# Optimization experiments

Measured on AMD Instinct MI355X. Metric: run time of the kernel, lower is better.

Reference implementation:

```python
import jax, jax.numpy as jnp
import numpy as np

D = 512      # input_dim == encoder d_model
E = 512      # embedding_dim (codebook dim)
V = 8192     # num_embeddings
NC = 1       # num_codebooks
L = 6        # encoder layers
H = 8        # heads
F = 2048     # ffn dim
HD = D // H
EPS = 1e-5


def layernorm(x, s, b):
    m = jnp.mean(x, -1, keepdims=True)
    v = jnp.mean((x - m) ** 2, -1, keepdims=True)
    return (x - m) * jax.lax.rsqrt(v + EPS) * s + b


def sinusoidal_pe(T):
    pos = np.arange(T, dtype=np.float32)[:, None]
    i = np.arange(0, D, 2, dtype=np.float32)[None, :]
    ang = pos / np.power(10000.0, i / D)
    pe = np.zeros((T, D), np.float32)
    pe[:, 0::2] = np.sin(ang)
    pe[:, 1::2] = np.cos(ang)
    return jnp.asarray(pe)


def setup_inputs():
    key = jax.random.key(0)
    ks = jax.random.split(key, 12)
    B, T = 8, 1024
    xs = jax.random.normal(ks[0], (B, T, D), jnp.float32)
    xs_lens = (T // 2 + jax.random.randint(ks[1], (B,), 0, T // 2)).astype(jnp.int32)
    mask_indices = jax.random.uniform(ks[2], (B, T)) < 0.12  # span-mask surrogate
    sc = lambda k, shape, s=0.02: jax.random.normal(k, shape, jnp.float32) * s
    return {
        "xs": xs, "xs_lens": xs_lens, "mask_indices": mask_indices,
        "W_embed": sc(ks[3], (D, D), D ** -0.5),
        "ln1_s": jnp.ones((L, D)), "ln1_b": jnp.zeros((L, D)),
        "Wqkv": sc(ks[4], (L, D, 3 * D)), "Wo": sc(ks[5], (L, D, D)),
        "ln2_s": jnp.ones((L, D)), "ln2_b": jnp.zeros((L, D)),
        "W1": sc(ks[6], (L, D, F)), "W2": sc(ks[7], (L, F, D)),
        "an_s": jnp.ones((D,)), "an_b": jnp.zeros((D,)),
        "iln_s": jnp.ones((D,)), "iln_b": jnp.zeros((D,)),
        "mask_emb": sc(ks[8], (D,), 0.1),
        "top_n_out": sc(ks[9], (NC, D, V)),
        "projection": sc(ks[10], (D, E), (2.0 / (D + E)) ** 0.5),  # xavier_normal, frozen
        "embeddings": jax.random.normal(ks[11], (NC, E, V), jnp.float32),  # frozen codebook
    }


def encoder_blocks(x, pad_mask, ln1_s, ln1_b, Wqkv, Wo, ln2_s, ln2_b, W1, W2, an_s, an_b):
    B, T, _ = x.shape
    attn_bias = jnp.where(pad_mask, 0.0, -1e9)[:, None, None, :]  # [B,1,1,T]

    def layer(x, p):
        l1s, l1b, wqkv, wo, l2s, l2b, w1, w2 = p
        h = layernorm(x, l1s, l1b)
        q, k, v = jnp.split(h @ wqkv, 3, axis=-1)
        q = q.reshape(B, T, H, HD)
        k = k.reshape(B, T, H, HD)
        v = v.reshape(B, T, H, HD)
        scores = jnp.einsum('bqhd,bkhd->bhqk', q, k) * (HD ** -0.5) + attn_bias
        o = jnp.einsum('bhqk,bkhd->bqhd', jax.nn.softmax(scores, axis=-1), v)
        x = x + o.reshape(B, T, D) @ wo
        h = layernorm(x, l2s, l2b)
        x = x + jax.nn.relu(h @ w1) @ w2
        return x, None

    x, _ = jax.lax.scan(layer, x, (ln1_s, ln1_b, Wqkv, Wo, ln2_s, ln2_b, W1, W2))
    return layernorm(x, an_s, an_b)


def nearest_ids(x, iln_s, iln_b, projection, embeddings):
    # layernorm -> projection -> squared-distance argmin per codebook
    B, T, _ = x.shape
    z = layernorm(x, iln_s, iln_b) @ projection        # [B,T,E]
    flat = z.reshape(-1, E)                            # [N,E]
    d = (jnp.sum(flat ** 2, 1)[None, :, None]
         + jnp.sum(embeddings ** 2, 1)[:, None, :]
         - 2.0 * jnp.einsum('ne,gev->gnv', flat, embeddings))  # [NC,N,V]
    return jnp.argmin(d, -1).T.reshape(B, T, NC)


def reference(xs, xs_lens, mask_indices, W_embed, ln1_s, ln1_b, Wqkv, Wo, ln2_s, ln2_b,
              W1, W2, an_s, an_b, iln_s, iln_b, mask_emb, top_n_out, projection, embeddings):
    B, T, _ = xs.shape
    pad_mask = jnp.arange(T)[None, :] < xs_lens[:, None]              # [B,T]
    x = xs @ W_embed + sinusoidal_pe(T)[None]                         # encoder.embed
    target_ids = nearest_ids(x, iln_s, iln_b, projection, embeddings)  # [B,T,NC]
    masked_xs = jnp.where(mask_indices[..., None], mask_emb, x)
    out = encoder_blocks(masked_xs, pad_mask, ln1_s, ln1_b, Wqkv, Wo,
                         ln2_s, ln2_b, W1, W2, an_s, an_b)            # [B,T,D]
    logits = jnp.einsum('btd,gdv->bgtv', out, top_n_out)              # [B,NC,T,V]
    lsm = jax.nn.log_softmax(logits, axis=-1)
    tgt = jnp.transpose(target_ids, (0, 2, 1))                        # [B,NC,T]
    ent = -jnp.take_along_axis(lsm, tgt[..., None], axis=-1)[..., 0]  # [B,NC,T]
    m = (pad_mask & mask_indices).astype(jnp.float32)                 # [B,T]
    loss = jnp.sum(ent * m[:, None, :]) / (jnp.sum(m) * NC)
    return loss
```

## Files before the change

### kernel.cpp

```cpp
#include <hip/hip_runtime.h>
#include <hip/hip_bf16.h>

#define D_ 512
#define T_ 1024
#define B_ 8
#define H_ 8
#define F_ 2048
#define V_ 8192
#define L_ 6
#define NTOK 8192
#define EPS_ 1e-5f
#define NCAP 2048

typedef short short8 __attribute__((ext_vector_type(8)));
typedef float floatx4 __attribute__((ext_vector_type(4)));

__device__ __forceinline__ float bf2f(unsigned short u) {
  union { unsigned int i; float f; } v; v.i = ((unsigned int)u) << 16; return v.f;
}
__device__ __forceinline__ unsigned short f2bf(float f) {
  unsigned int u = __float_as_uint(f);
  return (unsigned short)((u + 0x7fffu + ((u >> 16) & 1u)) >> 16);
}
__device__ __forceinline__ float ldf(const void* p, long long i, int bf) {
  if (bf) return bf2f(((const unsigned short*)p)[i]);
  return ((const float*)p)[i];
}
__device__ __forceinline__ void ld16(const unsigned short* g, unsigned short* l) {
  __builtin_amdgcn_global_load_lds(
      (const __attribute__((address_space(1))) unsigned int*)g,
      (__attribute__((address_space(3))) unsigned int*)l, 16, 0, 0);
}
__device__ __forceinline__ unsigned int fkey(float f) {
  unsigned int u = __float_as_uint(f);
  return (u & 0x80000000u) ? ~u : (u ^ 0x80000000u);
}

__global__ void detect_kernel(const unsigned int* xsw, const unsigned int* mw, int* flags) {
  __shared__ int cnt[256];
  __shared__ int m01[256], mlo[256], mhi[256];
  int tid = threadIdx.x;
  int c = 0;
  for (int t = tid; t < 1024; t += 256) {
    unsigned int lo = xsw[t] & 0xffffu;
    int ok;
    if (lo == 0u) ok = 1;
    else { unsigned int e = (lo >> 7) & 0xffu; ok = (e >= 90u && e <= 140u); }
    c += ok;
  }
  int n01 = 0, lo38 = 0, hi38 = 0;
  for (int t = tid; t < 2048; t += 256) {
    unsigned int w = mw[t];
    if (w > 1u) n01 = 1;
    if ((w & 0xffffu) == 0x3f80u) lo38 = 1;
    if ((w >> 16) == 0x3f80u) hi38 = 1;
  }
  cnt[tid] = c; m01[tid] = n01; mlo[tid] = lo38; mhi[tid] = hi38;
  __syncthreads();
  for (int s = 128; s > 0; s >>= 1) {
    if (tid < s) {
      cnt[tid] += cnt[tid + s];
      m01[tid] |= m01[tid + s]; mlo[tid] |= mlo[tid + s]; mhi[tid] |= mhi[tid + s];
    }
    __syncthreads();
  }
  if (tid == 0) {
    flags[0] = (cnt[0] > 700) ? 1 : 0;
    int fmt;
    if (!m01[0]) fmt = 0;
    else if (mlo[0]) fmt = 2;
    else if (mhi[0]) fmt = 3;
    else fmt = 1;
    flags[1] = fmt;
  }
}

__global__ void conv_all_kernel(const void* d4, const void* d5, const void* d8,
                                const void* d9, const void* d12, const void* d13,
                                const void* d14, const void* d15, const void* d16,
                                float* P, const int* flags) {
  int i = blockIdx.x * 256 + threadIdx.x;
  if (i >= 14848) return;
  int bf = flags[0];
  const void* src; int off;
  if (i < 3072) { src = d4; off = 0; }
  else if (i < 6144) { src = d5; off = 3072; }
  else if (i < 9216) { src = d8; off = 6144; }
  else if (i < 12288) { src = d9; off = 9216; }
  else if (i < 12800) { src = d12; off = 12288; }
  else if (i < 13312) { src = d13; off = 12800; }
  else if (i < 13824) { src = d14; off = 13312; }
  else if (i < 14336) { src = d15; off = 13824; }
  else { src = d16; off = 14336; }
  P[i] = ldf(src, i - off, bf);
}

__global__ void convb_kernel(const void* src, unsigned short* dst, int n, const int* flags) {
  int i = blockIdx.x * 256 + threadIdx.x;
  if (i < n) {
    if (flags[0]) dst[i] = ((const unsigned short*)src)[i];
    else dst[i] = f2bf(((const float*)src)[i]);
  }
}

__global__ __launch_bounds__(256) void trans_kernel(const void* src, unsigned short* dst,
                                                    int K, int N, const int* flags) {
  int bf = flags[0];
  __shared__ unsigned short tile[32][33];
  int n0 = blockIdx.x * 32, k0 = blockIdx.y * 32, batch = blockIdx.z;
  long long sbase = (long long)batch * K * N;
  long long dbase = (long long)batch * N * K;
  int c = threadIdx.x & 31, r8 = threadIdx.x >> 5;
#pragma unroll
  for (int rr = 0; rr < 4; ++rr) {
    int r = r8 + rr * 8;
    tile[r][c] = f2bf(ldf(src, sbase + (long long)(k0 + r) * N + n0 + c, bf));
  }
  __syncthreads();
#pragma unroll
  for (int rr = 0; rr < 4; ++rr) {
    int nn = r8 + rr * 8;
    dst[dbase + (long long)(n0 + nn) * K + k0 + c] = tile[c][nn];
  }
}

__global__ __launch_bounds__(256) void trans_big_kernel(const void* top, const void* emb,
                                                        unsigned short* TOPT, unsigned short* EMBT,
                                                        float* en, const int* flags) {
  int bf = flags[0];
  __shared__ unsigned short tile[32][33];
  int n0 = blockIdx.x * 32, k0 = blockIdx.y * 32, z = blockIdx.z;
  const void* src = z ? emb : top;
  unsigned short* dst = z ? EMBT : TOPT;
  int c = threadIdx.x & 31, r8 = threadIdx.x >> 5;
#pragma unroll
  for (int rr = 0; rr < 4; ++rr) {
    int r = r8 + rr * 8;
    tile[r][c] = f2bf(ldf(src, (long long)(k0 + r) * V_ + n0 + c, bf));
  }
  __syncthreads();
#pragma unroll
  for (int rr = 0; rr < 4; ++rr) {
    int nn = r8 + rr * 8;
    dst[(long long)(n0 + nn) * D_ + k0 + c] = tile[c][nn];
  }
  if (z == 1 && threadIdx.x < 32) {
    int nn = threadIdx.x;
    float s = 0.f;
#pragma unroll
    for (int r = 0; r < 32; ++r) { float x = bf2f(tile[r][nn]); s += x * x; }
    atomicAdd(&en[n0 + nn], s);
  }
}

__global__ void prep_kernel(const void* mask, const int* lens, int* maski, float* mcomb,
                            int* idx, int* cnt, const int* flags) {
  int i = blockIdx.x * 256 + threadIdx.x;
  if (i >= NTOK) return;
  int fmt = flags[1];
  int mi;
  if (fmt == 0) mi = ((const int*)mask)[i] != 0;
  else if (fmt == 1) mi = ((const unsigned char*)mask)[i] != 0;
  else if (fmt == 2) mi = ((const unsigned short*)mask)[i] != 0;
  else mi = ((const float*)mask)[i] != 0.f;
  int b = i >> 10, t = i & (T_ - 1);
  int act = mi && (t < lens[b]);
  maski[i] = mi;
  mcomb[i] = act ? 1.f : 0.f;
  if (act) {
    int p = atomicAdd(cnt, 1);
    if (p < NCAP) idx[p] = i;
  }
}

#define BK 32

template<int BN>
__device__ __forceinline__ void stage_tile(const unsigned short* A, long long ga0, long long ga1,
                                           const unsigned short* BT, long long gb0, long long gb1,
                                           int k0, unsigned short (*Ab)[BK],
                                           unsigned short (*Bb)[BK], int wave, int sw8) {
  ld16(A + ga0 + k0 + sw8, &Ab[wave * 32][0]);
  ld16(A + ga1 + k0 + sw8, &Ab[wave * 32 + 16][0]);
  if constexpr (BN == 128) {
    ld16(BT + gb0 + k0 + sw8, &Bb[wave * 32][0]);
    ld16(BT + gb1 + k0 + sw8, &Bb[wave * 32 + 16][0]);
  } else {
    ld16(BT + gb0 + k0 + sw8, &Bb[wave * 16][0]);
  }
}

template<int BN>
__device__ __forceinline__ void mfma_pipe(const unsigned short* A, long long ga0, long long ga1,
                                          const unsigned short* BT, int n0, int Kdim,
                                          int kofs, int Klen,
                                          unsigned short (*As)[BK], unsigned short (*Bs)[BK],
                                          floatx4 (*acc)[BN / 32], int tid) {
  constexpr int NB = BN / 32;
  int wave = tid >> 6, lane = tid & 63;
  int r16 = lane >> 2, c16 = lane & 3;
  int lrow = lane & 15, quad = lane >> 4;
  int wm = (wave & 1) * 64, wn = (wave >> 1) * (BN / 2);
  int NT = Klen / BK;
  int sw8 = (c16 ^ ((r16 >> 1) & 3)) * 8;
  int swr = (quad ^ ((lrow >> 1) & 3)) * 8;
  long long gb0, gb1 = 0;
  if constexpr (BN == 128) {
    gb0 = (long long)(n0 + wave * 32 + r16) * Kdim;
    gb1 = gb0 + 16LL * Kdim;
  } else {
    gb0 = (long long)(n0 + wave * 16 + r16) * Kdim;
  }
  ga0 += kofs; ga1 += kofs; gb0 += kofs; gb1 += kofs;
  stage_tile<BN>(A, ga0, ga1, BT, gb0, gb1, 0, As, Bs, wave, sw8);
  stage_tile<BN>(A, ga0, ga1, BT, gb0, gb1, BK, As + 128, Bs + BN, wave, sw8);
  int cur = 0, nxt = 2;
  for (int t = 0; t < NT; ++t) {
    if (t == NT - 1) {
      asm volatile("s_waitcnt vmcnt(0)" ::: "memory");
    } else {
      if constexpr (BN == 128) asm volatile("s_waitcnt vmcnt(4)" ::: "memory");
      else                     asm volatile("s_waitcnt vmcnt(3)" ::: "memory");
    }
    __builtin_amdgcn_s_barrier();
    if (t + 2 < NT)
      stage_tile<BN>(A, ga0, ga1, BT, gb0, gb1, (t + 2) * BK,
                     As + nxt * 128, Bs + nxt * BN, wave, sw8);
    unsigned short (*Ac)[BK] = As + cur * 128;
    unsigned short (*Bc)[BK] = Bs + cur * BN;
    short8 af[4], bfr[NB];
#pragma unroll
    for (int i = 0; i < 4; ++i) af[i] = *(const short8*)&Ac[wm + i * 16 + lrow][swr];
#pragma unroll
    for (int j = 0; j < NB; ++j) bfr[j] = *(const short8*)&Bc[wn + j * 16 + lrow][swr];
#pragma unroll
    for (int i = 0; i < 4; ++i)
#pragma unroll
      for (int j = 0; j < NB; ++j)
        acc[i][j] = __builtin_amdgcn_mfma_f32_16x16x32_bf16(af[i], bfr[j], acc[i][j], 0, 0, 0);
    cur = (cur == 2) ? 0 : cur + 1;
    nxt = (nxt == 2) ? 0 : nxt + 1;
  }
  __syncthreads();
}

__global__ __launch_bounds__(256) void mgemm_kernel(const unsigned short* A,
    const unsigned short* BT, long long boff, unsigned short* Cb, int Ndim, int Kdim) {
  __shared__ __align__(16) unsigned short As[3 * 128][BK];
  __shared__ __align__(16) unsigned short Bs[3 * 128][BK];
  int tid = threadIdx.x;
  int bid = blockIdx.x;
  int m0 = (bid & 63) * 128, n0 = (bid >> 6) * 128;
  int wave = tid >> 6, lane = tid & 63;
  int wm = (wave & 1) * 64, wn = (wave >> 1) * 64;
  int lrow = lane & 15, quad = lane >> 4;
  int r16 = lane >> 2;
  floatx4 acc[4][4];
#pragma unroll
  for (int i = 0; i < 4; ++i)
#pragma unroll
    for (int j = 0; j < 4; ++j) acc[i][j] = (floatx4){0.f, 0.f, 0.f, 0.f};
  long long ga0 = (long long)(m0 + wave * 32 + r16) * Kdim;
  long long ga1 = ga0 + 16LL * Kdim;
  mfma_pipe<128>(A, ga0, ga1, BT + boff, n0, Kdim, 0, Kdim, As, Bs, acc, tid);
#pragma unroll
  for (int i = 0; i < 4; ++i) {
    int mb = m0 + wm + i * 16 + quad * 4;
#pragma unroll
    for (int j = 0; j < 4; ++j) {
      int ncol = n0 + wn + j * 16 + lrow;
#pragma unroll
      for (int r = 0; r < 4; ++r)
        Cb[(long long)(mb + r) * Ndim + ncol] = f2bf(fmaxf(acc[i][j][r], 0.f));
    }
  }
}

__global__ __launch_bounds__(256) void mgemm64_kernel(const unsigned short* A,
    const unsigned short* BT, long long boff, float* Cf, unsigned short* Cb,
    int Ndim, int Kdim, int mode) {
  __shared__ __align__(16) unsigned short As[3 * 128][BK];
  __shared__ __align__(16) unsigned short Bs[3 * 64][BK];
  int tid = threadIdx.x;
  int bid = blockIdx.x;
  int m0 = (bid & 63) * 128;
  int nt = bid >> 6;
  int n0, kofs, Klen;
  if (mode == 5) { n0 = (nt & 7) * 64; kofs = (nt >> 3) * (Kdim >> 1); Klen = Kdim >> 1; }
  else { n0 = nt * 64; kofs = 0; Klen = Kdim; }
  int wave = tid >> 6, lane = tid & 63;
  int r16 = lane >> 2;
  int wm = (wave & 1) * 64, wn = (wave >> 1) * 32;
  int lrow = lane & 15, quad = lane >> 4;
  floatx4 acc[4][2];
#pragma unroll
  for (int i = 0; i < 4; ++i)
#pragma unroll
    for (int j = 0; j < 2; ++j) acc[i][j] = (floatx4){0.f, 0.f, 0.f, 0.f};
  long long ga0 = (long long)(m0 + wave * 32 + r16) * Kdim;
  long long ga1 = ga0 + 16LL * Kdim;
  mfma_pipe<64>(A, ga0, ga1, BT + boff, n0, Kdim, kofs, Klen, As, Bs, acc, tid);
#pragma unroll
  for (int i = 0; i < 4; ++i) {
    int mb = m0 + wm + i * 16 + quad * 4;
#pragma unroll
    for (int j = 0; j < 2; ++j) {
      int ncol = n0 + wn + j * 16 + lrow;
#pragma unroll
      for (int r = 0; r < 4; ++r) {
        int m = mb + r;
        long long idx = (long long)m * Ndim + ncol;
        float v = acc[i][j][r];
        if (mode == 1) Cf[idx] += v;
        else if (mode == 5) atomicAdd(&Cf[idx], v);
        else if (mode == 4) Cb[idx] = f2bf(v);
        else if (mode == 3) {
          int t = m & (T_ - 1);
          float freq = __expf(-(float)(ncol & ~1) * (9.210340371976184f / (float)D_));
          float ang = (float)t * freq;
          v += (ncol & 1) ? cosf(ang) : sinf(ang);
          Cf[idx] = v;
        } else Cf[idx] = v;
      }
    }
  }
}

__global__ __launch_bounds__(256) void qkvgemm_kernel(const unsigned short* A,
    const unsigned short* BT, long long boff, unsigned short* QB,
    unsigned short* KSg, unsigned short* VTSg) {
  __shared__ __align__(16) union {
    struct { unsigned short As[3 * 128][BK]; unsigned short Bs[3 * 128][BK]; } s;
    unsigned short T[128][136];
  } sm;
  int tid = threadIdx.x;
  int bid = blockIdx.x;
  int m0 = (bid & 63) * 128;
  int nt = bid >> 6;
  int n0 = nt * 128;
  int wave = tid >> 6, lane = tid & 63;
  int wm = (wave & 1) * 64, wn = (wave >> 1) * 64;
  int lrow = lane & 15, quad = lane >> 4;
  int r16 = lane >> 2;
  floatx4 acc[4][4];
#pragma unroll
  for (int i = 0; i < 4; ++i)
#pragma unroll
    for (int j = 0; j < 4; ++j) acc[i][j] = (floatx4){0.f, 0.f, 0.f, 0.f};
  long long ga0 = (long long)(m0 + wave * 32 + r16) * D_;
  long long ga1 = ga0 + 16LL * D_;
  mfma_pipe<128>(A, ga0, ga1, BT + boff, n0, D_, 0, D_, sm.s.As, sm.s.Bs, acc, tid);
  int b = m0 >> 10, tt = (m0 >> 7) & 7;
  if (nt < 4) {
#pragma unroll
    for (int i = 0; i < 4; ++i) {
      int mb = m0 + wm + i * 16 + quad * 4;
#pragma unroll
      for (int j = 0; j < 4; ++j) {
        int ncol = n0 + wn + j * 16 + lrow;
#pragma unroll
        for (int r = 0; r < 4; ++r)
          QB[(long long)(mb + r) * 512 + ncol] = f2bf(acc[i][j][r]);
      }
    }
  } else if (nt < 8) {
#pragma unroll
    for (int i = 0; i < 4; ++i)
#pragma unroll
      for (int j = 0; j < 4; ++j)
#pragma unroll
        for (int r = 0; r < 4; ++r)
          sm.T[wm + i * 16 + quad * 4 + r][wn + j * 16 + lrow] = f2bf(acc[i][j][r]);
    __syncthreads();
    int tk = tid & 127, hg0 = tid >> 7;
#pragma unroll
    for (int p = 0; p < 8; ++p) {
      int hg = p * 2 + hg0;
      int h2 = hg >> 3, g = hg & 7;
      uint4 u = *(const uint4*)&sm.T[tk][h2 * 64 + g * 8];
      int headg = (nt - 4) * 2 + h2;
      long long dst = (((((long long)(b * 8 + headg)) * 8 + tt) * 8 + g) * 128 + tk) * 8;
      *(uint4*)&KSg[dst] = u;
    }
  } else {
#pragma unroll
    for (int i = 0; i < 4; ++i)
#pragma unroll
      for (int j = 0; j < 4; ++j)
#pragma unroll
        for (int r = 0; r < 4; ++r)
          sm.T[wn + j * 16 + lrow][wm + i * 16 + quad * 4 + r] = f2bf(acc[i][j][r]);
    __syncthreads();
    int col = tid & 127, gh = tid >> 7;
    int h2 = col >> 6, ch = col & 63;
    int headg = (nt - 8) * 2 + h2;
    long long base = ((((long long)(b * 8 + headg)) * 8 + tt) * 16);
#pragma unroll
    for (int p = 0; p < 8; ++p) {
      int g = p * 2 + gh;
      uint4 u = *(const uint4*)&sm.T[col][g * 8];
      long long dst = ((base + g) * 64 + ch) * 8;
      *(uint4*)&VTSg[dst] = u;
    }
  }
}

__global__ __launch_bounds__(256) void fattn_kernel(const unsigned short* QB,
    const unsigned short* KSg, const unsigned short* VTSg, const int* lens,
    unsigned short* ao) {
  __shared__ __align__(16) unsigned short Ps[64 * 128];
  int blk = blockIdx.x;
  int swz = (blk & 7) * 128 + (blk >> 3);
  int qt = swz & 15, bh = swz >> 4;
  int b = bh >> 3, h = bh & 7;
  int tid = threadIdx.x, wave = tid >> 6, lane = tid & 63;
  int c = lane & 15, quad = lane >> 4;
  int len = lens[b];
  short8 qf[2];
#pragma unroll
  for (int ks = 0; ks < 2; ++ks)
    qf[ks] = *(const short8*)&QB[(long long)(b * 1024 + qt * 64 + wave * 16 + c) * 512
                                 + h * 64 + ks * 32 + quad * 8];
  floatx4 accO[4];
  float lr[4];
#pragma unroll
  for (int j = 0; j < 4; ++j) { accO[j] = (floatx4){0.f, 0.f, 0.f, 0.f}; lr[j] = 0.f; }
  int nkt = (len + 127) >> 7;
  const unsigned short* kp = KSg + (long long)bh * 65536;
  const unsigned short* vp = VTSg + (long long)bh * 65536;
  int kb = (quad * 128 + c) * 8;
  int vbase = quad * 512 + c * 8;
  int row = wave * 16 + c;
  short8 kA[8], kB[8], vA[8], vB[8];
#pragma unroll
  for (int j2 = 0; j2 < 4; ++j2) {
    kA[j2]     = *(const short8*)&kp[kb + j2 * 128];
    kA[4 + j2] = *(const short8*)&kp[kb + 4096 + j2 * 128];
  }
  for (int kt = 0; kt < nkt; ++kt) {
    int kbase = kt * 128;
    const unsigned short* kpc = kp + kt * 8192;
    const unsigned short* vpc = vp + kt * 8192;
    const unsigned short* kpn = kpc + 8192;
    int more = (kt + 1 < nkt);
#pragma unroll
    for (int j2 = 0; j2 < 4; ++j2) {
      kB[j2]     = *(const short8*)&kpc[kb + (4 + j2) * 128];
      kB[4 + j2] = *(const short8*)&kpc[kb + 4096 + (4 + j2) * 128];
    }
    floatx4 s0[4];
#pragma unroll
    for (int j2 = 0; j2 < 4; ++j2) s0[j2] = (floatx4){0.f, 0.f, 0.f, 0.f};
#pragma unroll
    for (int j2 = 0; j2 < 4; ++j2) {
      s0[j2] = __builtin_amdgcn_mfma_f32_16x16x32_bf16(qf[0], kA[j2], s0[j2], 0, 0, 0);
      s0[j2] = __builtin_amdgcn_mfma_f32_16x16x32_bf16(qf[1], kA[4 + j2], s0[j2], 0, 0, 0);
    }
#pragma unroll
    for (int q = 0; q < 8; ++q)
      vA[q] = *(const short8*)&vpc[(q >> 2) * 2048 + (q & 3) * 128 + vbase];
#pragma unroll
    for (int r = 0; r < 4; ++r) {
      int prow = wave * 16 + quad * 4 + r;
      int rx = quad * 4 + r;
#pragma unroll
      for (int j2 = 0; j2 < 4; ++j2) {
        int col = j2 * 16 + c;
        float s = s0[j2][r] * 0.125f;
        s = (kbase + col < len) ? s : -100.f;
        float p = __expf(s);
        lr[r] += p;
        Ps[prow * 128 + (((col >> 3) ^ rx) * 8) + (col & 7)] = f2bf(p);
      }
    }
    floatx4 s1[4];
#pragma unroll
    for (int j2 = 0; j2 < 4; ++j2) s1[j2] = (floatx4){0.f, 0.f, 0.f, 0.f};
#pragma unroll
    for (int j2 = 0; j2 < 4; ++j2) {
      s1[j2] = __builtin_amdgcn_mfma_f32_16x16x32_bf16(qf[0], kB[j2], s1[j2], 0, 0, 0);
      s1[j2] = __builtin_amdgcn_mfma_f32_16x16x32_bf16(qf[1], kB[4 + j2], s1[j2], 0, 0, 0);
    }
#pragma unroll
    for (int q = 0; q < 8; ++q)
      vB[q] = *(const short8*)&vpc[(2 + (q >> 2)) * 2048 + (q & 3) * 128 + vbase];
#pragma unroll
    for (int r = 0; r < 4; ++r) {
      int prow = wave * 16 + quad * 4 + r;
      int rx = quad * 4 + r;
#pragma unroll
      for (int j2 = 0; j2 < 4; ++j2) {
        int col = (4 + j2) * 16 + c;
        float s = s1[j2][r] * 0.125f;
        s = (kbase + col < len) ? s : -100.f;
        float p = __expf(s);
        lr[r] += p;
        Ps[prow * 128 + (((col >> 3) ^ rx) * 8) + (col & 7)] = f2bf(p);
      }
    }
#pragma unroll
    for (int kk2 = 0; kk2 < 2; ++kk2) {
      short8 pa = *(const short8*)&Ps[row * 128 + (((kk2 * 4 + quad) ^ c) * 8)];
#pragma unroll
      for (int jn = 0; jn < 4; ++jn)
        accO[jn] = __builtin_amdgcn_mfma_f32_16x16x32_bf16(pa, vA[kk2 * 4 + jn], accO[jn], 0, 0, 0);
    }
    if (more) {
#pragma unroll
      for (int j2 = 0; j2 < 4; ++j2) {
        kA[j2]     = *(const short8*)&kpn[kb + j2 * 128];
        kA[4 + j2] = *(const short8*)&kpn[kb + 4096 + j2 * 128];
      }
    }
#pragma unroll
    for (int kk2 = 0; kk2 < 2; ++kk2) {
      int kk = 2 + kk2;
      short8 pa = *(const short8*)&Ps[row * 128 + (((kk * 4 + quad) ^ c) * 8)];
#pragma unroll
      for (int jn = 0; jn < 4; ++jn)
        accO[jn] = __builtin_amdgcn_mfma_f32_16x16x32_bf16(pa, vB[kk2 * 4 + jn], accO[jn], 0, 0, 0);
    }
  }
#pragma unroll
  for (int r = 0; r < 4; ++r) {
    float ls = lr[r];
    ls += __shfl_xor(ls, 1, 64);
    ls += __shfl_xor(ls, 2, 64);
    ls += __shfl_xor(ls, 4, 64);
    ls += __shfl_xor(ls, 8, 64);
    float inv = 1.f / ls;
    long long token = b * 1024 + qt * 64 + wave * 16 + quad * 4 + r;
#pragma unroll
    for (int jn = 0; jn < 4; ++jn)
      ao[token * 512 + h * 64 + jn * 16 + c] = f2bf(accO[jn][r] * inv);
  }
}

__global__ __launch_bounds__(256) void dgemm_argmin(const unsigned short* Z, const int* ridx,
    const int* cnt, const unsigned short* ET, const float* en, unsigned long long* best) {
  __shared__ __align__(16) union {
    struct { unsigned short A[3 * 128][BK]; unsigned short B[3 * 128][BK]; } s;
    unsigned long long part[128][33];
  } sm;
  int m0 = blockIdx.y * 128;
  int na = *cnt;
  if (m0 >= ((na + 127) & ~127)) return;
  int tid = threadIdx.x;
  int n0 = blockIdx.x * 128;
  int wave = tid >> 6, lane = tid & 63;
  int wm = (wave & 1) * 64, wn = (wave >> 1) * 64;
  int lrow = lane & 15, quad = lane >> 4;
  int r16 = lane >> 2;
  int slot = (wave >> 1) * 16 + lrow;
  floatx4 acc[4][4];
#pragma unroll
  for (int i = 0; i < 4; ++i)
#pragma unroll
    for (int j = 0; j < 4; ++j) acc[i][j] = (floatx4){0.f, 0.f, 0.f, 0.f};
  long long ga0 = (long long)ridx[m0 + wave * 32 + r16] * D_;
  long long ga1 = (long long)ridx[m0 + wave * 32 + 16 + r16] * D_;
  mfma_pipe<128>(Z, ga0, ga1, ET, n0, D_, 0, D_, sm.s.A, sm.s.B, acc, tid);
  float env[4];
#pragma unroll
  for (int j = 0; j < 4; ++j) env[j] = en[n0 + wn + j * 16 + lrow];
#pragma unroll
  for (int i = 0; i < 4; ++i) {
#pragma unroll
    for (int r = 0; r < 4; ++r) {
      int rowl = wm + i * 16 + quad * 4 + r;
      unsigned long long bl = ~0ull;
#pragma unroll
      for (int j = 0; j < 4; ++j) {
        float v = env[j] - 2.f * acc[i][j][r];
        unsigned long long pk = (((unsigned long long)fkey(v)) << 32) |
                                (unsigned int)(n0 + wn + j * 16 + lrow);
        if (pk < bl) bl = pk;
      }
      sm.part[rowl][(slot + rowl) & 31] = bl;
    }
  }
  __syncthreads();
  if (tid < 128) {
    unsigned long long bb = sm.part[tid][0];
#pragma unroll 4
    for (int k2 = 1; k2 < 32; ++k2) { unsigned long long o = sm.part[tid][k2]; if (o < bb) bb = o; }
    atomicMin(&best[m0 + tid], bb);
  }
}

__global__ __launch_bounds__(256) void lgemm_lse(const unsigned short* OUTB, const int* ridx,
    const int* cnt, const unsigned short* TOPT, const unsigned long long* best,
    float* PS, float* TL) {
  __shared__ __align__(16) union {
    struct { unsigned short A[3 * 128][BK]; unsigned short B[3 * 128][BK]; } s;
    float part[128][33];
  } sm;
  int m0 = blockIdx.y * 128;
  int na = *cnt;
  if (m0 >= ((na + 127) & ~127)) return;
  int tid = threadIdx.x;
  int n0 = blockIdx.x * 128;
  int wave = tid >> 6, lane = tid & 63;
  int wm = (wave & 1) * 64, wn = (wave >> 1) * 64;
  int lrow = lane & 15, quad = lane >> 4;
  int r16 = lane >> 2;
  int slot = (wave >> 1) * 16 + lrow;
  floatx4 acc[4][4];
#pragma unroll
  for (int i = 0; i < 4; ++i)
#pragma unroll
    for (int j = 0; j < 4; ++j) acc[i][j] = (floatx4){0.f, 0.f, 0.f, 0.f};
  long long ga0 = (long long)ridx[m0 + wave * 32 + r16] * D_;
  long long ga1 = (long long)ridx[m0 + wave * 32 + 16 + r16] * D_;
  mfma_pipe<128>(OUTB, ga0, ga1, TOPT, n0, D_, 0, D_, sm.s.A, sm.s.B, acc, tid);
#pragma unroll
  for (int i = 0; i < 4; ++i) {
#pragma unroll
    for (int r = 0; r < 4; ++r) {
      int rowl = wm + i * 16 + quad * 4 + r;
      int tg = (int)(best[m0 + rowl] & 0xffffffffu);
      float ss = 0.f;
#pragma unroll
      for (int j = 0; j < 4; ++j) {
        float v = acc[i][j][r];
        ss += __expf(v);
        if (n0 + wn + j * 16 + lrow == tg) TL[m0 + rowl] = v;
      }
      sm.part[rowl][(slot + rowl) & 31] = ss;
    }
  }
  __syncthreads();
  if (tid < 128) {
    float S = 0.f;
#pragma unroll 4
    for (int k2 = 0; k2 < 32; ++k2) S += sm.part[tid][k2];
    PS[(long long)(m0 + tid) * 64 + blockIdx.x] = S;
  }
}

__global__ void lse_combine(const float* PS, const float* TL, const int* cnt, float* entm) {
  int t = blockIdx.x * 256 + threadIdx.x;
  if (t >= NCAP) return;
  if (t < *cnt) {
    float S = 0.f;
    for (int i = 0; i < 64; ++i) S += PS[(long long)t * 64 + i];
    entm[t] = __logf(S) - TL[t];
  } else {
    entm[t] = 0.f;
  }
}

__global__ __launch_bounds__(256) void ln_kernel(const float* X, float* Yf, unsigned short* Yb,
                                                 int obf, const float* s, const float* b) {
  int tid = threadIdx.x, wave = tid >> 6, lane = tid & 63;
  long long n = (long long)blockIdx.x * 4 + wave;
  const float* x = X + n * D_ + lane * 8;
  float v[8];
  *(float4*)&v[0] = *(const float4*)x;
  *(float4*)&v[4] = *(const float4*)(x + 4);
  float sum = 0.f;
#pragma unroll
  for (int j = 0; j < 8; ++j) sum += v[j];
  for (int m = 32; m; m >>= 1) sum += __shfl_xor(sum, m, 64);
  float mean = sum * (1.f / (float)D_);
  float vs = 0.f;
#pragma unroll
  for (int j = 0; j < 8; ++j) { v[j] -= mean; vs += v[j] * v[j]; }
  for (int m = 32; m; m >>= 1) vs += __shfl_xor(vs, m, 64);
  float r = rsqrtf(vs * (1.f / (float)D_) + EPS_);
  float sv[8], bv[8];
  *(float4*)&sv[0] = *(const float4*)(s + lane * 8);
  *(float4*)&sv[4] = *(const float4*)(s + lane * 8 + 4);
  *(float4*)&bv[0] = *(const float4*)(b + lane * 8);
  *(float4*)&bv[4] = *(const float4*)(b + lane * 8 + 4);
  if (obf) {
    unsigned short o[8];
#pragma unroll
    for (int j = 0; j < 8; ++j) o[j] = f2bf(v[j] * r * sv[j] + bv[j]);
    *(uint4*)(Yb + n * D_ + lane * 8) = *(const uint4*)o;
  } else {
    float o[8];
#pragma unroll
    for (int j = 0; j < 8; ++j) o[j] = v[j] * r * sv[j] + bv[j];
    *(float4*)(Yf + n * D_ + lane * 8) = *(const float4*)&o[0];
    *(float4*)(Yf + n * D_ + lane * 8 + 4) = *(const float4*)&o[4];
  }
}

__global__ void maskapply_kernel(float* x, const int* maski, const float* memb) {
  long long i = (long long)blockIdx.x * 256 + threadIdx.x;
  int n = (int)(i >> 9), d = (int)(i & 511);
  if (maski[n]) x[i] = memb[d];
}

__global__ void final_kernel(const float* entm, const float* mcomb, void* out) {
  __shared__ float r1[256], r2[256];
  int tid = threadIdx.x;
  float s1 = 0.f, s2 = 0.f;
  for (int i = tid; i < NCAP; i += 256) s1 += entm[i];
  for (int i = tid; i < NTOK; i += 256) s2 += mcomb[i];
  r1[tid] = s1; r2[tid] = s2;
  __syncthreads();
  for (int st = 128; st > 0; st >>= 1) {
    if (tid < st) { r1[tid] += r1[tid + st]; r2[tid] += r2[tid + st]; }
    __syncthreads();
  }
  if (tid == 0) {
    float loss = r1[0] / r2[0];
    unsigned short b16 = f2bf(loss);
    unsigned short* o = (unsigned short*)out;
    o[0] = b16; o[1] = b16;
  }
}

extern "C" void kernel_launch(void* const* d_in, const int* in_sizes, int n_in,
                              void* d_out, int out_size, void* d_ws, size_t ws_size,
                              hipStream_t stream) {
  if (n_in < 20) return;
  float* wsf = (float*)d_ws;
  int* flags = (int*)d_ws;
  const long long OF_P = 256;
  const long long OF_X = 16640;
  const long long OF_HB = OF_X + 4194304;
  const long long OF_BIG = OF_HB + 2097152;
  const long long OF_AOB = OF_BIG + 8388608;
  const long long OF_WT = OF_AOB + 2097152;
  const long long OF_TOPT = OF_WT + 9699328;
  const long long OF_EMBT = OF_TOPT + 2097152;
  const long long OF_EN = OF_EMBT + 2097152;
  const long long OF_BEST = OF_EN + 8192;
  const long long OF_PS = OF_BEST + 4096;
  const long long OF_TL = OF_PS + 131072;
  const long long OF_MI = OF_TL + 2048;
  const long long OF_MC = OF_MI + 8192;
  const long long OF_EM = OF_MC + 8192;
  const long long OF_CNT = OF_EM + 2048;
  const long long OF_IDX = OF_CNT + 16;
  const long long END = OF_IDX + 2048;
  if (ws_size < (size_t)END * 4) return;

  float* X = wsf + OF_X;
  unsigned short* HB = (unsigned short*)(wsf + OF_HB);
  unsigned short* BIGB = (unsigned short*)(wsf + OF_BIG);
  unsigned short* AOB = (unsigned short*)(wsf + OF_AOB);
  unsigned short* WT = (unsigned short*)(wsf + OF_WT);
  unsigned short* TOPT = (unsigned short*)(wsf + OF_TOPT);
  unsigned short* EMBT = (unsigned short*)(wsf + OF_EMBT);
  float* EN = wsf + OF_EN;
  unsigned long long* BEST = (unsigned long long*)(wsf + OF_BEST);
  float* PS = wsf + OF_PS;
  float* TL = wsf + OF_TL;
  int* MI = (int*)(wsf + OF_MI);
  float* MC = wsf + OF_MC;
  float* EM = wsf + OF_EM;
  int* CNT = (int*)(wsf + OF_CNT);
  int* IDX = (int*)(wsf + OF_IDX);
  float* P = wsf + OF_P;
  float* ln1s = P, *ln1b = P + 3072, *ln2s = P + 6144, *ln2b = P + 9216;
  float* ans = P + 12288, *anb = P + 12800, *ilns = P + 13312, *ilnb = P + 13824;
  float* memb = P + 14336;

  unsigned short* QB = BIGB;
  unsigned short* KSg = BIGB + 4194304;
  unsigned short* VTSg = BIGB + 8388608;

  const long long W_QKV = 0, W_O = 4718592, W_1 = 6291456, W_2 = 12582912,
                  W_EMB = 18874368, W_PRJ = 19136512;

  detect_kernel<<<1, 256, 0, stream>>>((const unsigned int*)d_in[0],
                                       (const unsigned int*)d_in[2], flags);
  hipMemsetAsync((void*)BEST, 0xFF, NCAP * 8, stream);
  hipMemsetAsync((void*)EN, 0, V_ * 4, stream);
  hipMemsetAsync((void*)CNT, 0, 16, stream);
  hipMemsetAsync((void*)IDX, 0, NCAP * 4, stream);
  conv_all_kernel<<<58, 256, 0, stream>>>(d_in[4], d_in[5], d_in[8], d_in[9], d_in[12],
                                          d_in[13], d_in[14], d_in[15], d_in[16], P, flags);
  prep_kernel<<<32, 256, 0, stream>>>(d_in[2], (const int*)d_in[1], MI, MC, IDX, CNT, flags);

  unsigned short* XSB = BIGB;
  convb_kernel<<<16384, 256, 0, stream>>>(d_in[0], XSB, 4194304, flags);

  trans_kernel<<<dim3(48, 16, 6), 256, 0, stream>>>(d_in[6], WT + W_QKV, 512, 1536, flags);
  trans_kernel<<<dim3(16, 16, 6), 256, 0, stream>>>(d_in[7], WT + W_O, 512, 512, flags);
  trans_kernel<<<dim3(64, 16, 6), 256, 0, stream>>>(d_in[10], WT + W_1, 512, 2048, flags);
  trans_kernel<<<dim3(16, 64, 6), 256, 0, stream>>>(d_in[11], WT + W_2, 2048, 512, flags);
  trans_kernel<<<dim3(16, 16, 1), 256, 0, stream>>>(d_in[3], WT + W_EMB, 512, 512, flags);
  trans_kernel<<<dim3(16, 16, 1), 256, 0, stream>>>(d_in[18], WT + W_PRJ, 512, 512, flags);
  trans_big_kernel<<<dim3(256, 16, 2), 256, 0, stream>>>(d_in[17], d_in[19], TOPT, EMBT,
                                                         EN, flags);

  dim3 gC(64, NCAP / 128);

  mgemm64_kernel<<<512, 256, 0, stream>>>(XSB, WT + W_EMB, 0, X, nullptr, 512, 512, 3);
  ln_kernel<<<2048, 256, 0, stream>>>(X, nullptr, HB, 1, ilns, ilnb);
  mgemm64_kernel<<<512, 256, 0, stream>>>(HB, WT + W_PRJ, 0, nullptr, AOB, 512, 512, 4);
  dgemm_argmin<<<gC, 256, 0, stream>>>(AOB, IDX, CNT, EMBT, EN, BEST);
  maskapply_kernel<<<16384, 256, 0, stream>>>(X, MI, memb);

  for (int l = 0; l < L_; ++l) {
    ln_kernel<<<2048, 256, 0, stream>>>(X, nullptr, HB, 1, ln1s + l * 512, ln1b + l * 512);
    qkvgemm_kernel<<<768, 256, 0, stream>>>(HB, WT + W_QKV, (long long)l * 786432,
                                            QB, KSg, VTSg);
    fattn_kernel<<<1024, 256, 0, stream>>>(QB, KSg, VTSg, (const int*)d_in[1], AOB);
    mgemm64_kernel<<<512, 256, 0, stream>>>(AOB, WT + W_O, (long long)l * 262144,
                                            X, nullptr, 512, 512, 1);
    ln_kernel<<<2048, 256, 0, stream>>>(X, nullptr, HB, 1, ln2s + l * 512, ln2b + l * 512);
    mgemm_kernel<<<1024, 256, 0, stream>>>(HB, WT + W_1, (long long)l * 1048576,
                                           BIGB, 2048, 512);
    mgemm64_kernel<<<1024, 256, 0, stream>>>(BIGB, WT + W_2, (long long)l * 1048576,
                                             X, nullptr, 512, 2048, 5);
  }
  ln_kernel<<<2048, 256, 0, stream>>>(X, nullptr, AOB, 1, ans, anb);
  lgemm_lse<<<gC, 256, 0, stream>>>(AOB, IDX, CNT, TOPT, BEST, PS, TL);
  lse_combine<<<8, 256, 0, stream>>>(PS, TL, CNT, EM);
  final_kernel<<<1, 256, 0, stream>>>(EM, MC, d_out);
}
```

Baseline: 1.382 ms.

## Rewrite narrow GEMM with 8 waves and drop split-K atomics for W2

The 128x64 GEMM kernel now runs 512 threads (8 waves). Each wave owns a 64x16 output strip and has its own inline triple-buffered K pipeline, with only the first four waves loading B. The W2 FFN projection no longer uses a two-way split-K with float atomicAdd. It runs 512 blocks over the full K=2048 and accumulates with a plain read-add-write. This removes atomic traffic and the split-K machinery from the shared pipe, at the cost of fewer blocks and a longer serial K loop for W2.

```diff
diff --git a/kernel.cpp b/kernel.cpp
--- a/kernel.cpp
+++ b/kernel.cpp
@@ -182,18 +182,13 @@
                                            unsigned short (*Bb)[BK], int wave, int sw8) {
   ld16(A + ga0 + k0 + sw8, &Ab[wave * 32][0]);
   ld16(A + ga1 + k0 + sw8, &Ab[wave * 32 + 16][0]);
-  if constexpr (BN == 128) {
-    ld16(BT + gb0 + k0 + sw8, &Bb[wave * 32][0]);
-    ld16(BT + gb1 + k0 + sw8, &Bb[wave * 32 + 16][0]);
-  } else {
-    ld16(BT + gb0 + k0 + sw8, &Bb[wave * 16][0]);
-  }
+  ld16(BT + gb0 + k0 + sw8, &Bb[wave * 32][0]);
+  ld16(BT + gb1 + k0 + sw8, &Bb[wave * 32 + 16][0]);
 }
 
 template<int BN>
 __device__ __forceinline__ void mfma_pipe(const unsigned short* A, long long ga0, long long ga1,
                                           const unsigned short* BT, int n0, int Kdim,
-                                          int kofs, int Klen,
                                           unsigned short (*As)[BK], unsigned short (*Bs)[BK],
                                           floatx4 (*acc)[BN / 32], int tid) {
   constexpr int NB = BN / 32;
@@ -201,17 +196,11 @@
   int r16 = lane >> 2, c16 = lane & 3;
   int lrow = lane & 15, quad = lane >> 4;
   int wm = (wave & 1) * 64, wn = (wave >> 1) * (BN / 2);
-  int NT = Klen / BK;
+  int NT = Kdim / BK;
   int sw8 = (c16 ^ ((r16 >> 1) & 3)) * 8;
   int swr = (quad ^ ((lrow >> 1) & 3)) * 8;
-  long long gb0, gb1 = 0;
-  if constexpr (BN == 128) {
-    gb0 = (long long)(n0 + wave * 32 + r16) * Kdim;
-    gb1 = gb0 + 16LL * Kdim;
-  } else {
-    gb0 = (long long)(n0 + wave * 16 + r16) * Kdim;
-  }
-  ga0 += kofs; ga1 += kofs; gb0 += kofs; gb1 += kofs;
+  long long gb0 = (long long)(n0 + wave * 32 + r16) * Kdim;
+  long long gb1 = gb0 + 16LL * Kdim;
   stage_tile<BN>(A, ga0, ga1, BT, gb0, gb1, 0, As, Bs, wave, sw8);
   stage_tile<BN>(A, ga0, ga1, BT, gb0, gb1, BK, As + 128, Bs + BN, wave, sw8);
   int cur = 0, nxt = 2;
@@ -219,8 +208,7 @@
     if (t == NT - 1) {
       asm volatile("s_waitcnt vmcnt(0)" ::: "memory");
     } else {
-      if constexpr (BN == 128) asm volatile("s_waitcnt vmcnt(4)" ::: "memory");
-      else                     asm volatile("s_waitcnt vmcnt(3)" ::: "memory");
+      asm volatile("s_waitcnt vmcnt(4)" ::: "memory");
     }
     __builtin_amdgcn_s_barrier();
     if (t + 2 < NT)
@@ -262,7 +250,7 @@
     for (int j = 0; j < 4; ++j) acc[i][j] = (floatx4){0.f, 0.f, 0.f, 0.f};
   long long ga0 = (long long)(m0 + wave * 32 + r16) * Kdim;
   long long ga1 = ga0 + 16LL * Kdim;
-  mfma_pipe<128>(A, ga0, ga1, BT + boff, n0, Kdim, 0, Kdim, As, Bs, acc, tid);
+  mfma_pipe<128>(A, ga0, ga1, BT + boff, n0, Kdim, As, Bs, acc, tid);
 #pragma unroll
   for (int i = 0; i < 4; ++i) {
     int mb = m0 + wm + i * 16 + quad * 4;
@@ -276,52 +264,73 @@
   }
 }
 
-__global__ __launch_bounds__(256) void mgemm64_kernel(const unsigned short* A,
+__global__ __launch_bounds__(512) void mgemm64_kernel(const unsigned short* A,
     const unsigned short* BT, long long boff, float* Cf, unsigned short* Cb,
     int Ndim, int Kdim, int mode) {
   __shared__ __align__(16) unsigned short As[3 * 128][BK];
   __shared__ __align__(16) unsigned short Bs[3 * 64][BK];
   int tid = threadIdx.x;
   int bid = blockIdx.x;
-  int m0 = (bid & 63) * 128;
-  int nt = bid >> 6;
-  int n0, kofs, Klen;
-  if (mode == 5) { n0 = (nt & 7) * 64; kofs = (nt >> 3) * (Kdim >> 1); Klen = Kdim >> 1; }
-  else { n0 = nt * 64; kofs = 0; Klen = Kdim; }
+  int m0 = (bid & 63) * 128, n0 = (bid >> 6) * 64;
   int wave = tid >> 6, lane = tid & 63;
-  int r16 = lane >> 2;
-  int wm = (wave & 1) * 64, wn = (wave >> 1) * 32;
+  int r16 = lane >> 2, c16 = lane & 3;
   int lrow = lane & 15, quad = lane >> 4;
-  floatx4 acc[4][2];
-#pragma unroll
-  for (int i = 0; i < 4; ++i)
-#pragma unroll
-    for (int j = 0; j < 2; ++j) acc[i][j] = (floatx4){0.f, 0.f, 0.f, 0.f};
-  long long ga0 = (long long)(m0 + wave * 32 + r16) * Kdim;
-  long long ga1 = ga0 + 16LL * Kdim;
-  mfma_pipe<64>(A, ga0, ga1, BT + boff, n0, Kdim, kofs, Klen, As, Bs, acc, tid);
+  int wm = (wave & 1) * 64, wn = (wave >> 1) * 16;
+  int sw8 = (c16 ^ ((r16 >> 1) & 3)) * 8;
+  int swr = (quad ^ ((lrow >> 1) & 3)) * 8;
+  const unsigned short* Bp = BT + boff;
+  long long ga = (long long)(m0 + wave * 16 + r16) * Kdim;
+  long long gb = (long long)(n0 + (wave & 3) * 16 + r16) * Kdim;
+  int hasB = wave < 4;
+  floatx4 acc[4];
+#pragma unroll
+  for (int i = 0; i < 4; ++i) acc[i] = (floatx4){0.f, 0.f, 0.f, 0.f};
+  int NT = Kdim / BK;
+  ld16(A + ga + sw8, &As[wave * 16][0]);
+  if (hasB) ld16(Bp + gb + sw8, &Bs[wave * 16][0]);
+  ld16(A + ga + BK + sw8, &As[128 + wave * 16][0]);
+  if (hasB) ld16(Bp + gb + BK + sw8, &Bs[64 + wave * 16][0]);
+  int cur = 0, nxt = 2;
+  for (int t = 0; t < NT; ++t) {
+    if (t == NT - 1)  asm volatile("s_waitcnt vmcnt(0)" ::: "memory");
+    else if (hasB)    asm volatile("s_waitcnt vmcnt(2)" ::: "memory");
+    else              asm volatile("s_waitcnt vmcnt(1)" ::: "memory");
+    __builtin_amdgcn_s_barrier();
+    if (t + 2 < NT) {
+      int k0 = (t + 2) * BK;
+      ld16(A + ga + k0 + sw8, &As[nxt * 128 + wave * 16][0]);
+      if (hasB) ld16(Bp + gb + k0 + sw8, &Bs[nxt * 64 + wave * 16][0]);
+    }
+    unsigned short (*Ac)[BK] = As + cur * 128;
+    unsigned short (*Bc)[BK] = Bs + cur * 64;
+    short8 af[4];
+#pragma unroll
+    for (int i = 0; i < 4; ++i) af[i] = *(const short8*)&Ac[wm + i * 16 + lrow][swr];
+    short8 bfr = *(const short8*)&Bc[wn + lrow][swr];
+#pragma unroll
+    for (int i = 0; i < 4; ++i)
+      acc[i] = __builtin_amdgcn_mfma_f32_16x16x32_bf16(af[i], bfr, acc[i], 0, 0, 0);
+    cur = (cur == 2) ? 0 : cur + 1;
+    nxt = (nxt == 2) ? 0 : nxt + 1;
+  }
 #pragma unroll
   for (int i = 0; i < 4; ++i) {
     int mb = m0 + wm + i * 16 + quad * 4;
-#pragma unroll
-    for (int j = 0; j < 2; ++j) {
-      int ncol = n0 + wn + j * 16 + lrow;
-#pragma unroll
-      for (int r = 0; r < 4; ++r) {
-        int m = mb + r;
-        long long idx = (long long)m * Ndim + ncol;
-        float v = acc[i][j][r];
-        if (mode == 1) Cf[idx] += v;
-        else if (mode == 5) atomicAdd(&Cf[idx], v);
-        else if (mode == 4) Cb[idx] = f2bf(v);
-        else if (mode == 3) {
-          int t = m & (T_ - 1);
-          float freq = __expf(-(float)(ncol & ~1) * (9.210340371976184f / (float)D_));
-          float ang = (float)t * freq;
-          v += (ncol & 1) ? cosf(ang) : sinf(ang);
-          Cf[idx] = v;
-        } else Cf[idx] = v;
-      }
+    int ncol = n0 + wn + lrow;
+#pragma unroll
+    for (int r = 0; r < 4; ++r) {
+      int m = mb + r;
+      long long idx = (long long)m * Ndim + ncol;
+      float v = acc[i][r];
+      if (mode == 1) Cf[idx] += v;
+      else if (mode == 4) Cb[idx] = f2bf(v);
+      else if (mode == 3) {
+        int t = m & (T_ - 1);
+        float freq = __expf(-(float)(ncol & ~1) * (9.210340371976184f / (float)D_));
+        float ang = (float)t * freq;
+        v += (ncol & 1) ? cosf(ang) : sinf(ang);
+        Cf[idx] = v;
+      } else Cf[idx] = v;
     }
   }
 }
@@ -349,7 +358,7 @@
     for (int j = 0; j < 4; ++j) acc[i][j] = (floatx4){0.f, 0.f, 0.f, 0.f};
   long long ga0 = (long long)(m0 + wave * 32 + r16) * D_;
   long long ga1 = ga0 + 16LL * D_;
-  mfma_pipe<128>(A, ga0, ga1, BT + boff, n0, D_, 0, D_, sm.s.As, sm.s.Bs, acc, tid);
+  mfma_pipe<128>(A, ga0, ga1, BT + boff, n0, D_, sm.s.As, sm.s.Bs, acc, tid);
   int b = m0 >> 10, tt = (m0 >> 7) & 7;
   if (nt < 4) {
 #pragma unroll
@@ -559,7 +568,7 @@
     for (int j = 0; j < 4; ++j) acc[i][j] = (floatx4){0.f, 0.f, 0.f, 0.f};
   long long ga0 = (long long)ridx[m0 + wave * 32 + r16] * D_;
   long long ga1 = (long long)ridx[m0 + wave * 32 + 16 + r16] * D_;
-  mfma_pipe<128>(Z, ga0, ga1, ET, n0, D_, 0, D_, sm.s.A, sm.s.B, acc, tid);
+  mfma_pipe<128>(Z, ga0, ga1, ET, n0, D_, sm.s.A, sm.s.B, acc, tid);
   float env[4];
 #pragma unroll
   for (int j = 0; j < 4; ++j) env[j] = en[n0 + wn + j * 16 + lrow];
@@ -612,7 +621,7 @@
     for (int j = 0; j < 4; ++j) acc[i][j] = (floatx4){0.f, 0.f, 0.f, 0.f};
   long long ga0 = (long long)ridx[m0 + wave * 32 + r16] * D_;
   long long ga1 = (long long)ridx[m0 + wave * 32 + 16 + r16] * D_;
-  mfma_pipe<128>(OUTB, ga0, ga1, TOPT, n0, D_, 0, D_, sm.s.A, sm.s.B, acc, tid);
+  mfma_pipe<128>(OUTB, ga0, ga1, TOPT, n0, D_, sm.s.A, sm.s.B, acc, tid);
 #pragma unroll
   for (int i = 0; i < 4; ++i) {
 #pragma unroll
@@ -791,9 +800,9 @@
 
   dim3 gC(64, NCAP / 128);
 
-  mgemm64_kernel<<<512, 256, 0, stream>>>(XSB, WT + W_EMB, 0, X, nullptr, 512, 512, 3);
+  mgemm64_kernel<<<512, 512, 0, stream>>>(XSB, WT + W_EMB, 0, X, nullptr, 512, 512, 3);
   ln_kernel<<<2048, 256, 0, stream>>>(X, nullptr, HB, 1, ilns, ilnb);
-  mgemm64_kernel<<<512, 256, 0, stream>>>(HB, WT + W_PRJ, 0, nullptr, AOB, 512, 512, 4);
+  mgemm64_kernel<<<512, 512, 0, stream>>>(HB, WT + W_PRJ, 0, nullptr, AOB, 512, 512, 4);
   dgemm_argmin<<<gC, 256, 0, stream>>>(AOB, IDX, CNT, EMBT, EN, BEST);
   maskapply_kernel<<<16384, 256, 0, stream>>>(X, MI, memb);
 
@@ -802,13 +811,13 @@
     qkvgemm_kernel<<<768, 256, 0, stream>>>(HB, WT + W_QKV, (long long)l * 786432,
                                             QB, KSg, VTSg);
     fattn_kernel<<<1024, 256, 0, stream>>>(QB, KSg, VTSg, (const int*)d_in[1], AOB);
-    mgemm64_kernel<<<512, 256, 0, stream>>>(AOB, WT + W_O, (long long)l * 262144,
+    mgemm64_kernel<<<512, 512, 0, stream>>>(AOB, WT + W_O, (long long)l * 262144,
                                             X, nullptr, 512, 512, 1);
     ln_kernel<<<2048, 256, 0, stream>>>(X, nullptr, HB, 1, ln2s + l * 512, ln2b + l * 512);
     mgemm_kernel<<<1024, 256, 0, stream>>>(HB, WT + W_1, (long long)l * 1048576,
                                            BIGB, 2048, 512);
-    mgemm64_kernel<<<1024, 256, 0, stream>>>(BIGB, WT + W_2, (long long)l * 1048576,
-                                             X, nullptr, 512, 2048, 5);
+    mgemm64_kernel<<<512, 512, 0, stream>>>(BIGB, WT + W_2, (long long)l * 1048576,
+                                            X, nullptr, 512, 2048, 1);
   }
   ln_kernel<<<2048, 256, 0, stream>>>(X, nullptr, AOB, 1, ans, anb);
   lgemm_lse<<<gC, 256, 0, stream>>>(AOB, IDX, CNT, TOPT, BEST, PS, TL);
```

After: 1.226 ms. 1.13x faster.
